# Kernel tuning notes

Hardware: AMD Instinct MI355X
Metric: run time of the kernel (lower is better)

The kernel has to match this reference:

```python
import jax, jax.numpy as jnp
import numpy as np

C = 1024
H = 16
DH = C // H
T = 2048
B = 2
EPS = 1e-5


def setup_inputs() -> dict:
    key = jax.random.key(0)
    ks = jax.random.split(key, 11)
    s = 1.0 / np.sqrt(C)
    return {
        "x": jax.random.normal(ks[0], (B, C, T), dtype=jnp.float32),
        "Wq": jax.random.normal(ks[1], (C, C), dtype=jnp.float32) * s,
        "bq": jax.random.normal(ks[2], (C,), dtype=jnp.float32) * 0.01,
        "Wk": jax.random.normal(ks[3], (C, C), dtype=jnp.float32) * s,
        "bk": jax.random.normal(ks[4], (C,), dtype=jnp.float32) * 0.01,
        "Wv": jax.random.normal(ks[5], (C, C), dtype=jnp.float32) * s,
        "bv": jax.random.normal(ks[6], (C,), dtype=jnp.float32) * 0.01,
        "Wo": jax.random.normal(ks[7], (C, C), dtype=jnp.float32) * s,
        "bo": jax.random.normal(ks[8], (C,), dtype=jnp.float32) * 0.01,
        "gamma": jax.random.normal(ks[9], (C,), dtype=jnp.float32) * 0.1,
        "beta": jax.random.normal(ks[10], (C,), dtype=jnp.float32) * 0.1,
    }


def reference(x, Wq, bq, Wk, bk, Wv, bv, Wo, bo, gamma, beta):
    scale = DH ** (-0.5)
    # conv1x1 projections: [B,C,T] x [C_out,C_in] -> [B,C,T]
    q = jnp.einsum('bct,dc->bdt', x, Wq) + bq[None, :, None]
    k = jnp.einsum('bct,dc->bdt', x, Wk) + bk[None, :, None]
    v = jnp.einsum('bct,dc->bdt', x, Wv) + bv[None, :, None]
    # split heads: [B,C,T] -> [B,H,Dh,T]
    q = q.reshape(B, H, DH, T).transpose(0, 1, 3, 2) * scale  # [B,H,T,Dh]
    k = k.reshape(B, H, DH, T)                                # [B,H,Dh,T]
    v = v.reshape(B, H, DH, T).transpose(0, 1, 3, 2)          # [B,H,T,Dh]
    sim = jnp.einsum('bhtd,bhds->bhts', q, k)                 # [B,H,T,T]
    attn = jax.nn.softmax(sim, axis=-1)
    attn = jnp.nan_to_num(attn, nan=0.0)
    out = jnp.einsum('bhts,bhsd->bhtd', attn, v)              # [B,H,T,Dh]
    out = out.transpose(0, 1, 3, 2).reshape(B, C, T)          # [B,C,T]
    y = jnp.einsum('bct,dc->bdt', out, Wo) + bo[None, :, None]
    # BatchNorm1d (training mode: batch statistics over B and T)
    mean = jnp.mean(y, axis=(0, 2), keepdims=True)
    var = jnp.var(y, axis=(0, 2), keepdims=True)
    y = (y - mean) * jax.lax.rsqrt(var + EPS)
    y = y * gamma[None, :, None] + beta[None, :, None]
    return x + y
```

## Files before the change

### kernel.cpp

```cpp
#include <hip/hip_runtime.h>

#define CC 1024
#define HH 16
#define DHH 64
#define TT 2048
#define BB 2

typedef short s8v __attribute__((ext_vector_type(8)));
typedef float f32x4 __attribute__((ext_vector_type(4)));

__device__ __forceinline__ unsigned short f2bf(float f) {
    union { float f; unsigned int u; } v; v.f = f;
    unsigned int r = v.u + 0x7FFFu + ((v.u >> 16) & 1u);
    return (unsigned short)(r >> 16);
}

__device__ __forceinline__ float fexp2(float x) {
#if __has_builtin(__builtin_amdgcn_exp2f)
    return __builtin_amdgcn_exp2f(x);
#else
    return exp2f(x);
#endif
}

__device__ __forceinline__ void gl_lds16(const unsigned short* g, unsigned short* l) {
    __builtin_amdgcn_global_load_lds(
        (const __attribute__((address_space(1))) unsigned int*)g,
        (__attribute__((address_space(3))) unsigned int*)l, 16, 0, 0);
}

__device__ __forceinline__ s8v lds_ld(const unsigned short* base, int byteoff) {
    return *(const s8v*)((const char*)base + byteoff);
}

__device__ __forceinline__ int xcd_swz(int orig, int nwg) {
    int cpx = nwg >> 3;
    return (orig & 7) * cpx + (orig >> 3);
}

__global__ void transpose_cast(const float* __restrict__ x, unsigned short* __restrict__ xT) {
    __shared__ float tile[32][33];
    int b = blockIdx.z;
    int t0 = blockIdx.x * 32, c0 = blockIdx.y * 32;
    int tx = threadIdx.x, ty = threadIdx.y;
    const float* xb = x + (size_t)b * CC * TT;
    #pragma unroll
    for (int i = 0; i < 32; i += 8)
        tile[ty + i][tx] = xb[(size_t)(c0 + ty + i) * TT + t0 + tx];
    __syncthreads();
    unsigned short* xTb = xT + (size_t)b * TT * CC;
    #pragma unroll
    for (int i = 0; i < 32; i += 8)
        xTb[(size_t)(t0 + ty + i) * CC + c0 + tx] = f2bf(tile[tx][ty + i]);
}

__global__ void cast_weights(const float* __restrict__ Wq, const float* __restrict__ Wk,
                             const float* __restrict__ Wv, const float* __restrict__ Wo,
                             unsigned short* __restrict__ out) {
    int i = blockIdx.x * 256 + threadIdx.x;
    int which = i >> 18;
    int j = (i & 0x3FFFF) * 4;
    const float* s = (which == 0) ? Wq : (which == 1) ? Wk : (which == 2) ? Wv : Wo;
    float4 v = *(const float4*)(s + j);
    unsigned short* d = out + (size_t)which * 1048576 + j;
    ushort4 pk; pk.x = f2bf(v.x); pk.y = f2bf(v.y); pk.z = f2bf(v.z); pk.w = f2bf(v.w);
    *(ushort4*)d = pk;
}

__device__ __forceinline__ void gemm_core_k1024(
    const unsigned short* __restrict__ A, const unsigned short* __restrict__ Bt,
    unsigned short* As, unsigned short* Bs,
    int m0, int n0, int tid, f32x4 (&acc)[4][4]) {
    const int w = tid >> 6, l = tid & 63;
    const int ln = l & 15, hi = l >> 4;
    const int wm = (w >> 1) * 64, wn = (w & 1) * 64;
    int offA[4], offB[4];
    #pragma unroll
    for (int i = 0; i < 4; ++i) {
        int ra = wm + 16 * i + ln;
        offA[i] = ra * 64 + ((hi ^ ((ra >> 1) & 3)) * 16);
        int rb = wn + 16 * i + ln;
        offB[i] = rb * 64 + ((hi ^ ((rb >> 1) & 3)) * 16);
    }
    const unsigned short* ap[2];
    const unsigned short* bp[2];
    #pragma unroll
    for (int j = 0; j < 2; ++j) {
        int p = j * 256 + tid;
        int r = p >> 2, g = (p & 3) ^ ((r >> 1) & 3);
        ap[j] = A + (size_t)(m0 + r) * CC + 8 * g;
        bp[j] = Bt + (size_t)(n0 + r) * CC + 8 * g;
    }
    auto stage = [&](int buf) {
        #pragma unroll
        for (int j = 0; j < 2; ++j) {
            gl_lds16(ap[j], As + buf * 4096 + (j * 256 + w * 64) * 8);
            gl_lds16(bp[j], Bs + buf * 4096 + (j * 256 + w * 64) * 8);
        }
        #pragma unroll
        for (int j = 0; j < 2; ++j) { ap[j] += 32; bp[j] += 32; }
    };
    stage(0);
    for (int kk = 0; kk < 32; ++kk) {
        const int cur = kk & 1;
        if (kk < 31) {
            stage(cur ^ 1);
            asm volatile("s_waitcnt vmcnt(4)" ::: "memory");
        } else {
            asm volatile("s_waitcnt vmcnt(0)" ::: "memory");
        }
        __builtin_amdgcn_sched_barrier(0);
        __builtin_amdgcn_s_barrier();
        __builtin_amdgcn_sched_barrier(0);
        const unsigned short* Ab = As + cur * 4096;
        const unsigned short* Bb = Bs + cur * 4096;
        s8v a[4], bb[4];
        #pragma unroll
        for (int i = 0; i < 4; ++i) { a[i] = lds_ld(Ab, offA[i]); bb[i] = lds_ld(Bb, offB[i]); }
        __builtin_amdgcn_s_setprio(1);
        #pragma unroll
        for (int i = 0; i < 4; ++i)
            #pragma unroll
            for (int jj = 0; jj < 4; ++jj)
                acc[i][jj] = __builtin_amdgcn_mfma_f32_16x16x32_bf16(a[i], bb[jj], acc[i][jj], 0, 0, 0);
        __builtin_amdgcn_s_setprio(0);
        __builtin_amdgcn_s_barrier();
        __builtin_amdgcn_sched_barrier(0);
    }
}

__global__ __launch_bounds__(256, 3)
void gemm_qkv(const unsigned short* __restrict__ xT, const unsigned short* __restrict__ Wb,
              unsigned short* __restrict__ qTp, unsigned short* __restrict__ kTp,
              unsigned short* __restrict__ vp,
              const float* __restrict__ bq, const float* __restrict__ bk,
              const float* __restrict__ bv, float qscale) {
    __shared__ unsigned short As[2 * 4096];
    __shared__ unsigned short Bs[2 * 4096];
    const int tid = threadIdx.x;
    const int wgid = xcd_swz(blockIdx.x, 768);
    const int z = wgid >> 7, bx = wgid & 127;
    const int which = z >> 1, b = z & 1;
    const long TC = (long)TT * CC;

    const unsigned short* A; const unsigned short* Bt;
    int m0, n0;
    if (which < 2) {
        A = xT + (size_t)b * TC;
        Bt = Wb + (size_t)which * 1048576;
        n0 = (bx & 7) * 128; m0 = (bx >> 3) * 128;
    } else {
        A = Wb + 2097152;
        Bt = xT + (size_t)b * TC;
        n0 = (bx & 15) * 128; m0 = (bx >> 4) * 128;
    }

    f32x4 acc[4][4] = {};
    gemm_core_k1024(A, Bt, As, Bs, m0, n0, tid, acc);

    const int w = tid >> 6, l = tid & 63;
    const int ln = l & 15, hi = l >> 4;
    const int wm = (w >> 1) * 64, wn = (w & 1) * 64;

    if (which < 2) {
        unsigned short* Out = (which == 0 ? qTp : kTp) + (size_t)b * TC;
        const float* bias = (which == 0) ? bq : bk;
        float scale = (which == 0) ? qscale : 1.0f;
        #pragma unroll
        for (int i = 0; i < 4; ++i)
            #pragma unroll
            for (int jj = 0; jj < 4; ++jj) {
                int col = n0 + wn + 16 * jj + ln;
                float bvv = bias[col];
                #pragma unroll
                for (int r = 0; r < 4; ++r) {
                    int row = m0 + wm + 16 * i + hi * 4 + r;
                    Out[(size_t)row * CC + col] = f2bf((acc[i][jj][r] + bvv) * scale);
                }
            }
    } else {
        unsigned short* Out = vp + (size_t)b * TC;
        #pragma unroll
        for (int i = 0; i < 4; ++i)
            #pragma unroll
            for (int r = 0; r < 4; ++r) {
                int row = m0 + wm + 16 * i + hi * 4 + r;
                float bvv = bv[row];
                #pragma unroll
                for (int jj = 0; jj < 4; ++jj) {
                    int col = n0 + wn + 16 * jj + ln;
                    Out[(size_t)row * TT + col] = f2bf(acc[i][jj][r] + bvv);
                }
            }
    }
}

__global__ __launch_bounds__(256, 2)
void gemm_y(const unsigned short* __restrict__ Wo, const unsigned short* __restrict__ outT,
            float* __restrict__ y, const float* __restrict__ bo) {
    __shared__ unsigned short As[2 * 4096];
    __shared__ unsigned short Bs[2 * 4096];
    const int tid = threadIdx.x;
    const int wgid = xcd_swz(blockIdx.x, 256);
    const int b = wgid >> 7, bx = wgid & 127;
    const int n0 = (bx & 15) * 128, m0 = (bx >> 4) * 128;
    const long TC = (long)TT * CC;

    f32x4 acc[4][4] = {};
    gemm_core_k1024(Wo, outT + (size_t)b * TC, As, Bs, m0, n0, tid, acc);

    const int w = tid >> 6, l = tid & 63;
    const int ln = l & 15, hi = l >> 4;
    const int wm = (w >> 1) * 64, wn = (w & 1) * 64;
    float* Out = y + (size_t)b * TC;
    #pragma unroll
    for (int i = 0; i < 4; ++i)
        #pragma unroll
        for (int r = 0; r < 4; ++r) {
            int row = m0 + wm + 16 * i + hi * 4 + r;
            float bvv = bo[row];
            #pragma unroll
            for (int jj = 0; jj < 4; ++jj) {
                int col = n0 + wn + 16 * jj + ln;
                Out[(size_t)row * TT + col] = acc[i][jj][r] + bvv;
            }
        }
}

__global__ __launch_bounds__(512, 4)
void attn_kernel(const unsigned short* __restrict__ qT,
                 const unsigned short* __restrict__ kT,
                 const unsigned short* __restrict__ vv,
                 unsigned short* __restrict__ oT) {
    __shared__ unsigned short Ks[2][128 * 64];
    __shared__ unsigned short Vs[2][64 * 128];

    const int tid = threadIdx.x;
    const int w = tid >> 6, l = tid & 63;
    const int ln = l & 15, hi = l >> 4;
    const int wgid = xcd_swz(blockIdx.x, 512);
    const int qt0 = (wgid & 15) * 128;
    const int bh = wgid >> 4;
    const int b = bh >> 4, h = bh & 15;
    const size_t bTT = (size_t)b * TT;

    const unsigned short* kp[2];
    const unsigned short* vp2[2];
    #pragma unroll
    for (int j = 0; j < 2; ++j) {
        int c = j * 512 + tid;
        int rk = c >> 3, gk = (c & 7) ^ (rk & 7);
        kp[j] = kT + (bTT + rk) * CC + h * DHH + 8 * gk;
        int rv = c >> 4, gv = (c & 15) ^ (rv & 7);
        vp2[j] = vv + ((size_t)b * CC + h * DHH + rv) * TT + 8 * gv;
    }
    auto stage = [&](int buf) {
        #pragma unroll
        for (int j = 0; j < 2; ++j)
            gl_lds16(kp[j], &Ks[buf][(j * 512 + w * 64) * 8]);
        #pragma unroll
        for (int j = 0; j < 2; ++j)
            gl_lds16(vp2[j], &Vs[buf][(j * 512 + w * 64) * 8]);
        #pragma unroll
        for (int j = 0; j < 2; ++j) { kp[j] += 128 * CC; vp2[j] += 128; }
    };

    stage(0);

    s8v qf[2];
    {
        const unsigned short* qbase = qT + (bTT + qt0 + w * 16 + ln) * CC + h * DHH;
        #pragma unroll
        for (int kc = 0; kc < 2; ++kc)
            qf[kc] = *(const s8v*)(qbase + kc * 32 + 8 * hi);
    }

    int koff[8][2];
    #pragma unroll
    for (int cf = 0; cf < 8; ++cf) {
        int rk = cf * 16 + ln;
        koff[cf][0] = rk * 128 + ((hi ^ (rk & 7)) * 16);
        koff[cf][1] = rk * 128 + (((4 + hi) ^ (rk & 7)) * 16);
    }

    f32x4 of[4] = {};
    float mi = -1e30f, li = 0.f;
    int fidx[4];
    #pragma unroll
    for (int r = 0; r < 4; ++r) fidx[r] = (l & 48) | (hi * 4 + r);

    for (int ti = 0; ti < 16; ++ti) {
        const int cur = ti & 1;
        if (ti < 15) {
            stage(cur ^ 1);
            asm volatile("s_waitcnt vmcnt(4)" ::: "memory");
        } else {
            asm volatile("s_waitcnt vmcnt(0)" ::: "memory");
        }
        __builtin_amdgcn_sched_barrier(0);
        __builtin_amdgcn_s_barrier();
        __builtin_amdgcn_sched_barrier(0);

        const unsigned short* Kb = &Ks[cur][0];
        const unsigned short* Vb = &Vs[cur][0];

        f32x4 sf[8];
        #pragma unroll
        for (int cf = 0; cf < 8; ++cf) {
            s8v k0 = lds_ld(Kb, koff[cf][0]);
            s8v k1 = lds_ld(Kb, koff[cf][1]);
            __builtin_amdgcn_s_setprio(1);
            f32x4 t = (f32x4){0.f, 0.f, 0.f, 0.f};
            t = __builtin_amdgcn_mfma_f32_16x16x32_bf16(k0, qf[0], t, 0, 0, 0);
            t = __builtin_amdgcn_mfma_f32_16x16x32_bf16(k1, qf[1], t, 0, 0, 0);
            sf[cf] = t;
            __builtin_amdgcn_s_setprio(0);
        }

        unsigned int pw[8][2];
        {
            float m4[8];
            #pragma unroll
            for (int cf = 0; cf < 8; ++cf)
                m4[cf] = fmaxf(fmaxf(sf[cf][0], sf[cf][1]), fmaxf(sf[cf][2], sf[cf][3]));
            float mx = fmaxf(fmaxf(fmaxf(m4[0], m4[1]), fmaxf(m4[2], m4[3])),
                             fmaxf(fmaxf(m4[4], m4[5]), fmaxf(m4[6], m4[7])));
            mx = fmaxf(mx, __shfl_xor(mx, 16));
            mx = fmaxf(mx, __shfl_xor(mx, 32));
            float fac = 1.0f;
            if (__any(mx > mi + 8.0f)) {
                float mn = fmaxf(mi, mx);
                fac = fexp2(mi - mn);
                mi = mn;
                float facr[4];
                #pragma unroll
                for (int r = 0; r < 4; ++r) facr[r] = __shfl(fac, fidx[r]);
                #pragma unroll
                for (int nf = 0; nf < 4; ++nf)
                    #pragma unroll
                    for (int r = 0; r < 4; ++r) of[nf][r] *= facr[r];
            }
            float mn = mi;
            float ps0 = 0.f, ps1 = 0.f, ps2 = 0.f, ps3 = 0.f;
            #pragma unroll
            for (int cf = 0; cf < 8; ++cf) {
                float p0 = fexp2(sf[cf][0] - mn);
                float p1 = fexp2(sf[cf][1] - mn);
                float p2 = fexp2(sf[cf][2] - mn);
                float p3 = fexp2(sf[cf][3] - mn);
                ps0 += p0; ps1 += p1; ps2 += p2; ps3 += p3;
                unsigned int w0, w1;
                asm("v_cvt_pk_bf16_f32 %0, %1, %2" : "=v"(w0) : "v"(p0), "v"(p1));
                asm("v_cvt_pk_bf16_f32 %0, %1, %2" : "=v"(w1) : "v"(p2), "v"(p3));
                pw[cf][0] = w0;
                pw[cf][1] = w1;
            }
            float ps = (ps0 + ps1) + (ps2 + ps3);
            ps += __shfl_xor(ps, 16);
            ps += __shfl_xor(ps, 32);
            li = li * fac + ps;
        }

        #pragma unroll
        for (int kc = 0; kc < 4; ++kc) {
            s8v pa;
            {
                unsigned int A0 = pw[2 * kc][0], B0 = pw[2 * kc + 1][0];
                unsigned int A1 = pw[2 * kc][1], B1 = pw[2 * kc + 1][1];
                asm("v_permlane32_swap_b32 %0, %1" : "+v"(A0), "+v"(B0));
                asm("v_permlane16_swap_b32 %0, %1" : "+v"(A0), "+v"(B0));
                asm("v_permlane32_swap_b32 %0, %1" : "+v"(A1), "+v"(B1));
                asm("v_permlane16_swap_b32 %0, %1" : "+v"(A1), "+v"(B1));
                union { unsigned int u[4]; s8v v; } up;
                up.u[0] = A0; up.u[1] = A1; up.u[2] = B0; up.u[3] = B1;
                pa = up.v;
            }
            __builtin_amdgcn_s_setprio(1);
            #pragma unroll
            for (int nf = 0; nf < 4; ++nf) {
                int rv = nf * 16 + ln;
                s8v vb = lds_ld(Vb, rv * 256 + (((kc * 4 + hi) ^ (rv & 7)) * 16));
                of[nf] = __builtin_amdgcn_mfma_f32_16x16x32_bf16(pa, vb, of[nf], 0, 0, 0);
            }
            __builtin_amdgcn_s_setprio(0);
        }
        __builtin_amdgcn_sched_barrier(0);
        __builtin_amdgcn_s_barrier();
        __builtin_amdgcn_sched_barrier(0);
    }

    {
        float inv = 1.0f / li;
        float invr[4];
        #pragma unroll
        for (int r = 0; r < 4; ++r) invr[r] = __shfl(inv, fidx[r]);
        #pragma unroll
        for (int nf = 0; nf < 4; ++nf)
            #pragma unroll
            for (int r = 0; r < 4; ++r) {
                int row = qt0 + w * 16 + hi * 4 + r;
                int col = h * DHH + nf * 16 + ln;
                oT[(bTT + row) * CC + col] = f2bf(of[nf][r] * invr[r]);
            }
    }
}

__global__ void bn_stats(const float* __restrict__ y, float* __restrict__ mean,
                         float* __restrict__ rstd) {
    int c = blockIdx.x;
    float s = 0.f, ss = 0.f;
    for (int b = 0; b < BB; ++b) {
        const float* row = y + ((size_t)b * CC + c) * TT;
        for (int t = threadIdx.x; t < TT; t += 256) {
            float v = row[t];
            s += v; ss += v * v;
        }
    }
    #pragma unroll
    for (int m = 1; m < 64; m <<= 1) { s += __shfl_xor(s, m); ss += __shfl_xor(ss, m); }
    __shared__ float a1[4], a2[4];
    int w = threadIdx.x >> 6;
    if ((threadIdx.x & 63) == 0) { a1[w] = s; a2[w] = ss; }
    __syncthreads();
    if (threadIdx.x == 0) {
        s = a1[0] + a1[1] + a1[2] + a1[3];
        ss = a2[0] + a2[1] + a2[2] + a2[3];
        const float inv_n = 1.0f / (BB * TT);
        float mu = s * inv_n;
        float var = ss * inv_n - mu * mu;
        mean[c] = mu;
        rstd[c] = rsqrtf(var + 1e-5f);
    }
}

__global__ void final_out(const float* __restrict__ x, const float* __restrict__ y,
                          const float* __restrict__ mean, const float* __restrict__ rstd,
                          const float* __restrict__ gamma, const float* __restrict__ beta,
                          float* __restrict__ out) {
    int row = blockIdx.x;
    int c = row & (CC - 1);
    float a = gamma[c] * rstd[c];
    float bb = beta[c] - mean[c] * a;
    size_t base = (size_t)row * TT;
    for (int t = threadIdx.x * 4; t < TT; t += 256 * 4) {
        float4 xv = *(const float4*)(x + base + t);
        float4 yv = *(const float4*)(y + base + t);
        float4 o;
        o.x = xv.x + a * yv.x + bb;
        o.y = xv.y + a * yv.y + bb;
        o.z = xv.z + a * yv.z + bb;
        o.w = xv.w + a * yv.w + bb;
        *(float4*)(out + base + t) = o;
    }
}

extern "C" void kernel_launch(void* const* d_in, const int* in_sizes, int n_in,
                              void* d_out, int out_size, void* d_ws, size_t ws_size,
                              hipStream_t stream) {
    const float* x     = (const float*)d_in[0];
    const float* Wq    = (const float*)d_in[1];
    const float* bq    = (const float*)d_in[2];
    const float* Wk    = (const float*)d_in[3];
    const float* bk    = (const float*)d_in[4];
    const float* Wv    = (const float*)d_in[5];
    const float* bv    = (const float*)d_in[6];
    const float* Wo    = (const float*)d_in[7];
    const float* bo    = (const float*)d_in[8];
    const float* gamma = (const float*)d_in[9];
    const float* beta  = (const float*)d_in[10];
    float* out = (float*)d_out;

    char* ws = (char*)d_ws;
    unsigned short* buf0 = (unsigned short*)(ws);
    unsigned short* Wb   = (unsigned short*)(ws + 8388608);
    unsigned short* qTp  = (unsigned short*)(ws + 16777216);
    unsigned short* kTp  = (unsigned short*)(ws + 25165824);
    unsigned short* vp   = (unsigned short*)(ws + 33554432);
    float* yp            = (float*)(ws + 16777216);
    float* meanp         = (float*)(ws + 41943040);
    float* rstdp         = (float*)(ws + 41947136);

    transpose_cast<<<dim3(TT / 32, CC / 32, BB), dim3(32, 8), 0, stream>>>(x, buf0);
    cast_weights<<<dim3(4096), dim3(256), 0, stream>>>(Wq, Wk, Wv, Wo, Wb);

    gemm_qkv<<<dim3(768), dim3(256), 0, stream>>>(
        buf0, Wb, qTp, kTp, vp, bq, bk, bv, 0.125f * 1.4426950408889634f);

    attn_kernel<<<dim3(512), dim3(512), 0, stream>>>(qTp, kTp, vp, buf0);

    gemm_y<<<dim3(256), dim3(256), 0, stream>>>(Wb + 3145728, buf0, yp, bo);

    bn_stats<<<dim3(CC), dim3(256), 0, stream>>>(yp, meanp, rstdp);
    final_out<<<dim3(BB * CC), dim3(256), 0, stream>>>(x, yp, meanp, rstdp, gamma, beta, out);
}
```

Before: 133.4 us.

## Triple-buffer GEMM loads, split gemm_y tiles, software-pipeline attention QK

The shared GEMM core becomes a three-stage LDS pipeline with a single barrier per k-step, replacing the double buffer that needed two barriers. gemm_y now uses 128x64 tiles and launches 512 blocks instead of 256 to fill more CUs. The attention loop is restructured so that the next tile's QK^T is computed right after the next K/V stage is issued, overlapping it with the softmax and PV work of the current tile. The cost is more LDS per block, which may lower occupancy, and a full vmcnt(0) wait in the attention loop that may expose load latency.

```diff
diff --git a/kernel.cpp b/kernel.cpp
--- a/kernel.cpp
+++ b/kernel.cpp
@@ -67,65 +67,87 @@
     *(ushort4*)d = pk;
 }
 
+template<int NFRAG>
 __device__ __forceinline__ void gemm_core_k1024(
     const unsigned short* __restrict__ A, const unsigned short* __restrict__ Bt,
     unsigned short* As, unsigned short* Bs,
-    int m0, int n0, int tid, f32x4 (&acc)[4][4]) {
+    int m0, int n0, int tid, f32x4 (&acc)[4][NFRAG]) {
     const int w = tid >> 6, l = tid & 63;
     const int ln = l & 15, hi = l >> 4;
-    const int wm = (w >> 1) * 64, wn = (w & 1) * 64;
-    int offA[4], offB[4];
+    const int wm = (w >> 1) * 64, wn = (w & 1) * (NFRAG * 16);
+    const int BSZ = NFRAG * 1024;
+    int offA[4], offB[NFRAG];
     #pragma unroll
     for (int i = 0; i < 4; ++i) {
         int ra = wm + 16 * i + ln;
         offA[i] = ra * 64 + ((hi ^ ((ra >> 1) & 3)) * 16);
-        int rb = wn + 16 * i + ln;
-        offB[i] = rb * 64 + ((hi ^ ((rb >> 1) & 3)) * 16);
+    }
+    #pragma unroll
+    for (int j = 0; j < NFRAG; ++j) {
+        int rb = wn + 16 * j + ln;
+        offB[j] = rb * 64 + ((hi ^ ((rb >> 1) & 3)) * 16);
     }
     const unsigned short* ap[2];
-    const unsigned short* bp[2];
+    const unsigned short* bp[NFRAG / 2];
     #pragma unroll
     for (int j = 0; j < 2; ++j) {
         int p = j * 256 + tid;
         int r = p >> 2, g = (p & 3) ^ ((r >> 1) & 3);
         ap[j] = A + (size_t)(m0 + r) * CC + 8 * g;
+    }
+    #pragma unroll
+    for (int j = 0; j < NFRAG / 2; ++j) {
+        int p = j * 256 + tid;
+        int r = p >> 2, g = (p & 3) ^ ((r >> 1) & 3);
         bp[j] = Bt + (size_t)(n0 + r) * CC + 8 * g;
     }
     auto stage = [&](int buf) {
         #pragma unroll
         for (int j = 0; j < 2; ++j) {
             gl_lds16(ap[j], As + buf * 4096 + (j * 256 + w * 64) * 8);
-            gl_lds16(bp[j], Bs + buf * 4096 + (j * 256 + w * 64) * 8);
-        }
-        #pragma unroll
-        for (int j = 0; j < 2; ++j) { ap[j] += 32; bp[j] += 32; }
+            ap[j] += 32;
+        }
+        #pragma unroll
+        for (int j = 0; j < NFRAG / 2; ++j) {
+            gl_lds16(bp[j], Bs + buf * BSZ + (j * 256 + w * 64) * 8);
+            bp[j] += 32;
+        }
     };
-    stage(0);
+    stage(0); stage(1); stage(2);
+    if constexpr (NFRAG == 4) asm volatile("s_waitcnt vmcnt(8)" ::: "memory");
+    else                      asm volatile("s_waitcnt vmcnt(6)" ::: "memory");
+    __builtin_amdgcn_sched_barrier(0);
+    __builtin_amdgcn_s_barrier();
+    __builtin_amdgcn_sched_barrier(0);
+    int buf = 0;
     for (int kk = 0; kk < 32; ++kk) {
-        const int cur = kk & 1;
-        if (kk < 31) {
-            stage(cur ^ 1);
-            asm volatile("s_waitcnt vmcnt(4)" ::: "memory");
-        } else {
-            asm volatile("s_waitcnt vmcnt(0)" ::: "memory");
-        }
-        __builtin_amdgcn_sched_barrier(0);
-        __builtin_amdgcn_s_barrier();
-        __builtin_amdgcn_sched_barrier(0);
-        const unsigned short* Ab = As + cur * 4096;
-        const unsigned short* Bb = Bs + cur * 4096;
-        s8v a[4], bb[4];
-        #pragma unroll
-        for (int i = 0; i < 4; ++i) { a[i] = lds_ld(Ab, offA[i]); bb[i] = lds_ld(Bb, offB[i]); }
+        const unsigned short* Ab = As + buf * 4096;
+        const unsigned short* Bb = Bs + buf * BSZ;
+        s8v a[4], bb[NFRAG];
+        #pragma unroll
+        for (int i = 0; i < 4; ++i) a[i] = lds_ld(Ab, offA[i]);
+        #pragma unroll
+        for (int j = 0; j < NFRAG; ++j) bb[j] = lds_ld(Bb, offB[j]);
         __builtin_amdgcn_s_setprio(1);
         #pragma unroll
         for (int i = 0; i < 4; ++i)
             #pragma unroll
-            for (int jj = 0; jj < 4; ++jj)
+            for (int jj = 0; jj < NFRAG; ++jj)
                 acc[i][jj] = __builtin_amdgcn_mfma_f32_16x16x32_bf16(a[i], bb[jj], acc[i][jj], 0, 0, 0);
         __builtin_amdgcn_s_setprio(0);
-        __builtin_amdgcn_s_barrier();
-        __builtin_amdgcn_sched_barrier(0);
+        if (kk < 31) {
+            if (kk < 29) {
+                if constexpr (NFRAG == 4) asm volatile("s_waitcnt vmcnt(4)" ::: "memory");
+                else                      asm volatile("s_waitcnt vmcnt(3)" ::: "memory");
+            } else {
+                asm volatile("s_waitcnt vmcnt(0)" ::: "memory");
+            }
+            __builtin_amdgcn_sched_barrier(0);
+            __builtin_amdgcn_s_barrier();
+            __builtin_amdgcn_sched_barrier(0);
+            if (kk < 29) stage(buf);
+            buf = (buf == 2) ? 0 : buf + 1;
+        }
     }
 }
 
@@ -135,8 +157,8 @@
               unsigned short* __restrict__ vp,
               const float* __restrict__ bq, const float* __restrict__ bk,
               const float* __restrict__ bv, float qscale) {
-    __shared__ unsigned short As[2 * 4096];
-    __shared__ unsigned short Bs[2 * 4096];
+    __shared__ unsigned short As[3 * 4096];
+    __shared__ unsigned short Bs[3 * 4096];
     const int tid = threadIdx.x;
     const int wgid = xcd_swz(blockIdx.x, 768);
     const int z = wgid >> 7, bx = wgid & 127;
@@ -156,7 +178,7 @@
     }
 
     f32x4 acc[4][4] = {};
-    gemm_core_k1024(A, Bt, As, Bs, m0, n0, tid, acc);
+    gemm_core_k1024<4>(A, Bt, As, Bs, m0, n0, tid, acc);
 
     const int w = tid >> 6, l = tid & 63;
     const int ln = l & 15, hi = l >> 4;
@@ -198,20 +220,20 @@
 __global__ __launch_bounds__(256, 2)
 void gemm_y(const unsigned short* __restrict__ Wo, const unsigned short* __restrict__ outT,
             float* __restrict__ y, const float* __restrict__ bo) {
-    __shared__ unsigned short As[2 * 4096];
-    __shared__ unsigned short Bs[2 * 4096];
+    __shared__ unsigned short As[3 * 4096];
+    __shared__ unsigned short Bs[3 * 2048];
     const int tid = threadIdx.x;
-    const int wgid = xcd_swz(blockIdx.x, 256);
-    const int b = wgid >> 7, bx = wgid & 127;
-    const int n0 = (bx & 15) * 128, m0 = (bx >> 4) * 128;
+    const int wgid = xcd_swz(blockIdx.x, 512);
+    const int b = wgid >> 8, bx = wgid & 255;
+    const int n0 = (bx & 31) * 64, m0 = (bx >> 5) * 128;
     const long TC = (long)TT * CC;
 
-    f32x4 acc[4][4] = {};
-    gemm_core_k1024(Wo, outT + (size_t)b * TC, As, Bs, m0, n0, tid, acc);
+    f32x4 acc[4][2] = {};
+    gemm_core_k1024<2>(Wo, outT + (size_t)b * TC, As, Bs, m0, n0, tid, acc);
 
     const int w = tid >> 6, l = tid & 63;
     const int ln = l & 15, hi = l >> 4;
-    const int wm = (w >> 1) * 64, wn = (w & 1) * 64;
+    const int wm = (w >> 1) * 64, wn = (w & 1) * 32;
     float* Out = y + (size_t)b * TC;
     #pragma unroll
     for (int i = 0; i < 4; ++i)
@@ -220,7 +242,7 @@
             int row = m0 + wm + 16 * i + hi * 4 + r;
             float bvv = bo[row];
             #pragma unroll
-            for (int jj = 0; jj < 4; ++jj) {
+            for (int jj = 0; jj < 2; ++jj) {
                 int col = n0 + wn + 16 * jj + ln;
                 Out[(size_t)row * TT + col] = acc[i][jj][r] + bvv;
             }
@@ -266,6 +288,7 @@
     };
 
     stage(0);
+    stage(1);
 
     s8v qf[2];
     {
@@ -284,27 +307,19 @@
     }
 
     f32x4 of[4] = {};
+    f32x4 sf[8];
     float mi = -1e30f, li = 0.f;
     int fidx[4];
     #pragma unroll
     for (int r = 0; r < 4; ++r) fidx[r] = (l & 48) | (hi * 4 + r);
 
-    for (int ti = 0; ti < 16; ++ti) {
-        const int cur = ti & 1;
-        if (ti < 15) {
-            stage(cur ^ 1);
-            asm volatile("s_waitcnt vmcnt(4)" ::: "memory");
-        } else {
-            asm volatile("s_waitcnt vmcnt(0)" ::: "memory");
-        }
-        __builtin_amdgcn_sched_barrier(0);
-        __builtin_amdgcn_s_barrier();
-        __builtin_amdgcn_sched_barrier(0);
-
-        const unsigned short* Kb = &Ks[cur][0];
-        const unsigned short* Vb = &Vs[cur][0];
-
-        f32x4 sf[8];
+    asm volatile("s_waitcnt vmcnt(4)" ::: "memory");
+    __builtin_amdgcn_sched_barrier(0);
+    __builtin_amdgcn_s_barrier();
+    __builtin_amdgcn_sched_barrier(0);
+
+    auto qk = [&](int buf) {
+        const unsigned short* Kb = &Ks[buf][0];
         #pragma unroll
         for (int cf = 0; cf < 8; ++cf) {
             s8v k0 = lds_ld(Kb, koff[cf][0]);
@@ -316,8 +331,12 @@
             sf[cf] = t;
             __builtin_amdgcn_s_setprio(0);
         }
-
-        unsigned int pw[8][2];
+    };
+
+    qk(0);
+
+    unsigned int pw[8][2];
+    for (int ti = 0; ti < 16; ++ti) {
         {
             float m4[8];
             #pragma unroll
@@ -361,32 +380,41 @@
             li = li * fac + ps;
         }
 
-        #pragma unroll
-        for (int kc = 0; kc < 4; ++kc) {
-            s8v pa;
-            {
-                unsigned int A0 = pw[2 * kc][0], B0 = pw[2 * kc + 1][0];
-                unsigned int A1 = pw[2 * kc][1], B1 = pw[2 * kc + 1][1];
-                asm("v_permlane32_swap_b32 %0, %1" : "+v"(A0), "+v"(B0));
-                asm("v_permlane16_swap_b32 %0, %1" : "+v"(A0), "+v"(B0));
-                asm("v_permlane32_swap_b32 %0, %1" : "+v"(A1), "+v"(B1));
-                asm("v_permlane16_swap_b32 %0, %1" : "+v"(A1), "+v"(B1));
-                union { unsigned int u[4]; s8v v; } up;
-                up.u[0] = A0; up.u[1] = A1; up.u[2] = B0; up.u[3] = B1;
-                pa = up.v;
-            }
-            __builtin_amdgcn_s_setprio(1);
-            #pragma unroll
-            for (int nf = 0; nf < 4; ++nf) {
-                int rv = nf * 16 + ln;
-                s8v vb = lds_ld(Vb, rv * 256 + (((kc * 4 + hi) ^ (rv & 7)) * 16));
-                of[nf] = __builtin_amdgcn_mfma_f32_16x16x32_bf16(pa, vb, of[nf], 0, 0, 0);
-            }
-            __builtin_amdgcn_s_setprio(0);
-        }
-        __builtin_amdgcn_sched_barrier(0);
-        __builtin_amdgcn_s_barrier();
-        __builtin_amdgcn_sched_barrier(0);
+        {
+            const unsigned short* Vb = &Vs[ti & 1][0];
+            #pragma unroll
+            for (int kc = 0; kc < 4; ++kc) {
+                s8v pa;
+                {
+                    unsigned int A0 = pw[2 * kc][0], B0 = pw[2 * kc + 1][0];
+                    unsigned int A1 = pw[2 * kc][1], B1 = pw[2 * kc + 1][1];
+                    asm("v_permlane32_swap_b32 %0, %1" : "+v"(A0), "+v"(B0));
+                    asm("v_permlane16_swap_b32 %0, %1" : "+v"(A0), "+v"(B0));
+                    asm("v_permlane32_swap_b32 %0, %1" : "+v"(A1), "+v"(B1));
+                    asm("v_permlane16_swap_b32 %0, %1" : "+v"(A1), "+v"(B1));
+                    union { unsigned int u[4]; s8v v; } up;
+                    up.u[0] = A0; up.u[1] = A1; up.u[2] = B0; up.u[3] = B1;
+                    pa = up.v;
+                }
+                __builtin_amdgcn_s_setprio(1);
+                #pragma unroll
+                for (int nf = 0; nf < 4; ++nf) {
+                    int rv = nf * 16 + ln;
+                    s8v vb = lds_ld(Vb, rv * 256 + (((kc * 4 + hi) ^ (rv & 7)) * 16));
+                    of[nf] = __builtin_amdgcn_mfma_f32_16x16x32_bf16(pa, vb, of[nf], 0, 0, 0);
+                }
+                __builtin_amdgcn_s_setprio(0);
+            }
+        }
+
+        if (ti < 15) {
+            asm volatile("s_waitcnt vmcnt(0)" ::: "memory");
+            __builtin_amdgcn_sched_barrier(0);
+            __builtin_amdgcn_s_barrier();
+            __builtin_amdgcn_sched_barrier(0);
+            if (ti < 14) stage(ti & 1);
+            qk((ti + 1) & 1);
+        }
     }
 
     {
@@ -488,7 +516,7 @@
 
     attn_kernel<<<dim3(512), dim3(512), 0, stream>>>(qTp, kTp, vp, buf0);
 
-    gemm_y<<<dim3(256), dim3(256), 0, stream>>>(Wb + 3145728, buf0, yp, bo);
+    gemm_y<<<dim3(512), dim3(256), 0, stream>>>(Wb + 3145728, buf0, yp, bo);
 
     bn_stats<<<dim3(CC), dim3(256), 0, stream>>>(yp, meanp, rstdp);
     final_out<<<dim3(BB * CC), dim3(256), 0, stream>>>(x, yp, meanp, rstdp, gamma, beta, out);
```

Result: no change. 132.1 us (-1.0%).
